# Performance work log

Measured on AMD Instinct MI355X. Metric: run time of the kernel, lower is better.

## Reference

```python
import jax, jax.numpy as jnp
import numpy as np

EPS = 1e-5
D_MODEL = 128; D_INNER = 256; D_STATE = 64; D_CONV = 4; NHEADS = 8; HEADDIM = 32
N_LAYERS = 4; PATCH = 16; IMG = 512; BATCH = 16
D_IN_PROJ = 2 * D_INNER + 2 * D_STATE + NHEADS  # 648
CONV_DIM = D_INNER + 2 * D_STATE               # 384


def _layernorm(x, g, b):
    m = jnp.mean(x, -1, keepdims=True)
    v = jnp.mean((x - m) ** 2, -1, keepdims=True)
    return (x - m) * jax.lax.rsqrt(v + EPS) * g + b


def _mamba2(x, in_w, conv_w, conv_b, dt_bias, A_log, D_skip, norm_w, out_w):
    # x: (b, l, d_model). Faithful to mamba-ssm Mamba2 (ngroups=1, rmsnorm gated, D skip).
    b, l, _ = x.shape
    zxbcdt = jnp.einsum('bld,ed->ble', x, in_w)            # (b,l,648)
    z = zxbcdt[..., :D_INNER]
    xBC = zxbcdt[..., D_INNER:D_INNER + CONV_DIM]
    dt = zxbcdt[..., -NHEADS:]
    # causal depthwise conv1d (kernel D_CONV) + SiLU
    xpad = jnp.pad(xBC, ((0, 0), (D_CONV - 1, 0), (0, 0)))
    xc = conv_b + sum(xpad[:, k:k + l, :] * conv_w[:, k] for k in range(D_CONV))
    xc = jax.nn.silu(xc)
    xs = xc[..., :D_INNER]
    B = xc[..., D_INNER:D_INNER + D_STATE]                 # (b,l,n)
    C = xc[..., -D_STATE:]                                 # (b,l,n)
    dt = jax.nn.softplus(dt + dt_bias)                     # (b,l,h)
    dA = jnp.exp(dt * (-jnp.exp(A_log)))                   # (b,l,h)
    xh = xs.reshape(b, l, NHEADS, HEADDIM)                 # (b,l,h,p)

    def step(hstate, t):
        dA_t, dt_t, B_t, x_t, C_t = t
        hstate = hstate * dA_t[:, :, None, None] + jnp.einsum('bh,bn,bhp->bhpn', dt_t, B_t, x_t)
        return hstate, jnp.einsum('bhpn,bn->bhp', hstate, C_t)

    h0 = jnp.zeros((b, NHEADS, HEADDIM, D_STATE), x.dtype)
    _, ys = jax.lax.scan(step, h0, (dA.swapaxes(0, 1), dt.swapaxes(0, 1), B.swapaxes(0, 1), xh.swapaxes(0, 1), C.swapaxes(0, 1)))
    y = ys.swapaxes(0, 1) + D_skip[None, None, :, None] * xh
    y = y.reshape(b, l, D_INNER)
    y = y * jax.nn.silu(z)                                 # gate
    y = y * jax.lax.rsqrt(jnp.mean(y * y, -1, keepdims=True) + EPS) * norm_w  # gated RMSNorm
    return jnp.einsum('ble,de->bld', y, out_w)


def _forward(x, patch_w, patch_b, pe_g, pe_b, in_w, conv_w, conv_b, dt_bias, A_log,
             D_skip, ssm_norm_w, out_w, ln_g, ln_b, fn_g, fn_b, attn_w1, attn_b1, attn_w2, attn_b2):
    b = x.shape[0]
    Hp = x.shape[2] // PATCH; Wp = x.shape[3] // PATCH
    # patch-embed conv (stride==kernel) as a reshape + einsum
    xp = x.reshape(b, 3, Hp, PATCH, Wp, PATCH)
    tok = jnp.einsum('bchpwq,dcpq->bhwd', xp, patch_w) + patch_b
    tok = tok.reshape(b, Hp * Wp, D_MODEL)
    tok = _layernorm(tok, pe_g, pe_b)
    for i in range(N_LAYERS):
        res = tok
        tok = _layernorm(tok, ln_g[i], ln_b[i])
        tok = _mamba2(tok, in_w[i], conv_w[i], conv_b[i], dt_bias[i], A_log[i],
                      D_skip[i], ssm_norm_w[i], out_w[i])
        tok = tok + res
    tok = _layernorm(tok, fn_g, fn_b)
    # attention pooling
    h1 = jnp.tanh(jnp.einsum('bld,hd->blh', tok, attn_w1) + attn_b1)
    scores = jnp.einsum('blh,oh->blo', h1, attn_w2) + attn_b2
    w = jax.nn.softmax(scores, axis=1)
    pooled = jnp.sum(w * tok, axis=1)
    nrm = jnp.maximum(jnp.sqrt(jnp.sum(pooled * pooled, -1, keepdims=True)), 1e-12)
    return pooled / nrm


def setup_inputs() -> dict:
    key = jax.random.key(0)
    ks = jax.random.split(key, 16)
    n = lambda k, shape, s=0.02: (jax.random.normal(k, shape) * s).astype(jnp.float32)
    return {
        'x': jax.random.normal(ks[0], (BATCH, 3, IMG, IMG), jnp.float32),
        'patch_w': n(ks[1], (D_MODEL, 3, PATCH, PATCH)),
        'patch_b': jnp.zeros((D_MODEL,), jnp.float32),
        'pe_g': jnp.ones((D_MODEL,), jnp.float32),
        'pe_b': jnp.zeros((D_MODEL,), jnp.float32),
        'in_w': n(ks[2], (N_LAYERS, D_IN_PROJ, D_MODEL)),
        'conv_w': n(ks[3], (N_LAYERS, CONV_DIM, D_CONV), 0.1),
        'conv_b': jnp.zeros((N_LAYERS, CONV_DIM), jnp.float32),
        'dt_bias': n(ks[4], (N_LAYERS, NHEADS), 0.5),
        'A_log': jnp.log(jax.random.uniform(ks[5], (N_LAYERS, NHEADS), jnp.float32, 1.0, 16.0)),
        'D_skip': jnp.ones((N_LAYERS, NHEADS), jnp.float32),
        'ssm_norm_w': jnp.ones((N_LAYERS, D_INNER), jnp.float32),
        'out_w': n(ks[6], (N_LAYERS, D_MODEL, D_INNER)),
        'ln_g': jnp.ones((N_LAYERS, D_MODEL), jnp.float32),
        'ln_b': jnp.zeros((N_LAYERS, D_MODEL), jnp.float32),
        'fn_g': jnp.ones((D_MODEL,), jnp.float32),
        'fn_b': jnp.zeros((D_MODEL,), jnp.float32),
        'attn_w1': n(ks[7], (D_MODEL // 2, D_MODEL), 0.05),
        'attn_b1': jnp.zeros((D_MODEL // 2,), jnp.float32),
        'attn_w2': n(ks[8], (1, D_MODEL // 2), 0.05),
        'attn_b2': jnp.zeros((1,), jnp.float32),
    }


def reference(x, patch_w, patch_b, pe_g, pe_b, in_w, conv_w, conv_b, dt_bias, A_log,
              D_skip, ssm_norm_w, out_w, ln_g, ln_b, fn_g, fn_b, attn_w1, attn_b1, attn_w2, attn_b2):
    return _forward(x, patch_w, patch_b, pe_g, pe_b, in_w, conv_w, conv_b, dt_bias, A_log,
                    D_skip, ssm_norm_w, out_w, ln_g, ln_b, fn_g, fn_b, attn_w1, attn_b1, attn_w2, attn_b2)
```

## Files before the change

kernel.cpp:

```cpp
#include <hip/hip_runtime.h>
#include <math.h>

#define EPS 1e-5f

constexpr int NB      = 16;
constexpr int L       = 1024;
constexpr int DM      = 128;
constexpr int DI      = 256;
constexpr int DS      = 64;
constexpr int NH      = 8;
constexpr int DPROJ   = 648;
constexpr int CDIM    = 384;
constexpr int EPAD    = 656;

typedef __attribute__((ext_vector_type(8))) short short8v;
typedef __attribute__((ext_vector_type(4))) float f32x4;
typedef unsigned short ushort_t;

__device__ __forceinline__ float silu_f(float x){ return x / (1.f + expf(-x)); }
__device__ __forceinline__ ushort_t f2bf(float f){
  union { float f; unsigned int u; } v; v.f = f;
  unsigned int r = v.u + 0x7FFF + ((v.u >> 16) & 1);
  return (ushort_t)(r >> 16);
}
__device__ __forceinline__ short8v pack8(float4 a, float4 b){
  short8v v;
  v[0]=(short)f2bf(a.x); v[1]=(short)f2bf(a.y); v[2]=(short)f2bf(a.z); v[3]=(short)f2bf(a.w);
  v[4]=(short)f2bf(b.x); v[5]=(short)f2bf(b.y); v[6]=(short)f2bf(b.z); v[7]=(short)f2bf(b.w);
  return v;
}

__global__ __launch_bounds__(256) void k_cvt(const float* __restrict__ in_w,
    const float* __restrict__ ln_g, const float* __restrict__ ln_b,
    const float* __restrict__ out_w, const float* __restrict__ nw,
    const float* __restrict__ patch_w, const float* __restrict__ w1,
    ushort_t* __restrict__ inwb, ushort_t* __restrict__ owb,
    ushort_t* __restrict__ pwb, float* __restrict__ biasin,
    ushort_t* __restrict__ w1b){
  const int R1 = 4 * EPAD * 128, R2 = 4 * 128 * 256, R3 = 128 * 768, R4 = 4 * EPAD, R5 = 64 * 128;
  int i = blockIdx.x * 256 + threadIdx.x;
  if (i < R1) {
    int ly = i / (EPAD * 128), rem = i % (EPAD * 128), e = rem >> 7, d = rem & 127;
    float v = 0.f;
    if (e < DPROJ) v = in_w[((size_t)ly * DPROJ + e) * 128 + d] * ln_g[ly * 128 + d];
    inwb[i] = f2bf(v);
    return;
  }
  i -= R1;
  if (i < R2) {
    int ly = i >> 15, rem = i & 32767, e = rem & 255;
    owb[i] = f2bf(out_w[i] * nw[ly * 256 + e]);
    return;
  }
  i -= R2;
  if (i < R3) { pwb[i] = f2bf(patch_w[i]); return; }
  i -= R3;
  if (i < R4) {
    int ly = i / EPAD, e = i % EPAD;
    float s = 0.f;
    if (e < DPROJ) {
      const float* r = in_w + ((size_t)ly * DPROJ + e) * 128;
      const float* b = ln_b + ly * 128;
      for (int d = 0; d < 128; ++d) s += r[d] * b[d];
    }
    biasin[i] = s;
    return;
  }
  i -= R4;
  if (i < R5) w1b[i] = f2bf(w1[i]);
}

__global__ __launch_bounds__(256) void k_patch(const float* __restrict__ x,
    const ushort_t* __restrict__ pwb, const float* __restrict__ pb,
    const float* __restrict__ pg, const float* __restrict__ pbe,
    float* __restrict__ tok){
  __shared__ ushort_t Al[64 * 128];
  __shared__ ushort_t Bl[128 * 128];
  __shared__ float spb[128], spg[128], spe[128];
  const int m0 = blockIdx.x * 64;
  const int tid = threadIdx.x;
  char* Ab = (char*)Al; char* Bb = (char*)Bl;
  if (tid < 128) { spb[tid] = pb[tid]; spg[tid] = pg[tid]; spe[tid] = pbe[tid]; }
  const int w = tid >> 6, l = tid & 63, lr = l & 15, lgp = l >> 4;
  f32x4 acc[8];
#pragma unroll
  for (int nt = 0; nt < 8; ++nt) acc[nt] = (f32x4){0.f, 0.f, 0.f, 0.f};
  for (int kc = 0; kc < 6; ++kc) {
    __syncthreads();
    for (int idx = tid; idx < 128 * 16; idx += 256) {
      int n = idx >> 4, ch = idx & 15;
      short8v v = *(const short8v*)(pwb + (size_t)n * 768 + kc * 128 + (ch << 3));
      *(short8v*)(Bb + n * 256 + ((ch * 16) ^ ((n & 7) << 4))) = v;
    }
    {
      const int c = kc >> 1;
      for (int i = tid; i < 1024; i += 256) {
        int t = i >> 4, p = (i >> 1) & 7, o = i & 1;
        int T = m0 + t, bb = T >> 10, tl = T & 1023, hp = tl >> 5, wp = tl & 31;
        const float* src = x + (((size_t)(bb * 3 + c) * 512 + hp * 16 + ((kc & 1) << 3) + p) * 512
                                + wp * 16 + o * 8);
        float4 f0 = *(const float4*)src;
        float4 f1 = *(const float4*)(src + 4);
        short8v v = pack8(f0, f1);
        int kk = p * 16 + o * 8;
        *(short8v*)(Ab + t * 256 + ((kk * 2) ^ ((t & 7) << 4))) = v;
      }
// ... 39 lines not shown
      tok[row + col] = (v - mean) * rstd * spg[col] + spe[col];
    }
  }
}

__global__ __launch_bounds__(256) void k_inproj(const float* __restrict__ tok,
    const ushort_t* __restrict__ inwb, const float* __restrict__ biasin,
    float* __restrict__ zx){
  __shared__ ushort_t Al[128 * 128];
  __shared__ ushort_t Bl[176 * 128];
  __shared__ float sBias[176];
  const int blk = blockIdx.x;
  const int mb = blk >> 2, nb = blk & 3;
  const int m0 = mb << 7, n0 = nb * 176;
  const int NT = (nb == 3) ? 128 : 176;
  const int tid = threadIdx.x;
  char* Ab = (char*)Al; char* Bb = (char*)Bl;
  for (int idx = tid; idx < (NT << 4); idx += 256) {
    int row = idx >> 4, ch = idx & 15;
    short8v v = *(const short8v*)(inwb + ((size_t)(n0 + row) << 7) + (ch << 3));
    *(short8v*)(Bb + row * 256 + ((ch * 16) ^ ((row & 7) << 4))) = v;
  }
  for (int idx = tid; idx < NT; idx += 256) sBias[idx] = biasin[n0 + idx];
  for (int rp = 0; rp < 2; ++rp) {
    const int r = (rp << 6) + (tid >> 2), t4 = tid & 3;
    const float* src = tok + (((size_t)(m0 + r)) << 7) + t4 * 32;
    float v[32];
    float s = 0.f, sq = 0.f;
#pragma unroll
    for (int k = 0; k < 8; ++k) {
      float4 f = *(const float4*)(src + 4 * k);
      v[4*k] = f.x; v[4*k+1] = f.y; v[4*k+2] = f.z; v[4*k+3] = f.w;
      s += f.x + f.y + f.z + f.w;
      sq += f.x*f.x + f.y*f.y + f.z*f.z + f.w*f.w;
    }
    s  += __shfl_xor(s, 1, 4);  s  += __shfl_xor(s, 2, 4);
    sq += __shfl_xor(sq, 1, 4); sq += __shfl_xor(sq, 2, 4);
    float mean = s * (1.f / 128.f);
    float var  = sq * (1.f / 128.f) - mean * mean;
    float rstd = rsqrtf(var + EPS);
#pragma unroll
    for (int k = 0; k < 4; ++k) {
      short8v o;
#pragma unroll
      for (int e = 0; e < 8; ++e) o[e] = (short)f2bf((v[8*k + e] - mean) * rstd);
      *(short8v*)(Ab + r * 256 + ((t4 * 64 + 16 * k) ^ ((r & 7) << 4))) = o;
    }
  }
  __syncthreads();
  const int w = tid >> 6, l = tid & 63, lr = l & 15, lgp = l >> 4;
  const int xsl = (lr & 7) << 4;
  short8v a[2][4];
#pragma unroll
  for (int mi = 0; mi < 2; ++mi) {
    const int mt = w + mi * 4;
#pragma unroll
    for (int ks = 0; ks < 4; ++ks)
      a[mi][ks] = *(const short8v*)(Ab + (16 * mt + lr) * 256 + ((ks * 64 + lgp * 16) ^ xsl));
  }
  const int NTT = NT >> 4;
  for (int nt = 0; nt < NTT; ++nt) {
    f32x4 acc0 = (f32x4){0.f, 0.f, 0.f, 0.f};
    f32x4 acc1 = (f32x4){0.f, 0.f, 0.f, 0.f};
#pragma unroll
    for (int ks = 0; ks < 4; ++ks) {
      short8v b = *(const short8v*)(Bb + (nt * 16 + lr) * 256 + ((ks * 64 + lgp * 16) ^ xsl));
      acc0 = __builtin_amdgcn_mfma_f32_16x16x32_bf16(a[0][ks], b, acc0, 0, 0, 0);
      acc1 = __builtin_amdgcn_mfma_f32_16x16x32_bf16(a[1][ks], b, acc1, 0, 0, 0);
    }
    const int col = n0 + nt * 16 + lr;
    if (col < DPROJ) {
      const float bias = sBias[nt * 16 + lr];
#pragma unroll
      for (int r = 0; r < 4; ++r) {
        zx[((size_t)(m0 + 16 * w       + lgp * 4 + r)) * DPROJ + col] = acc0[r] + bias;
        zx[((size_t)(m0 + 16 * (w + 4) + lgp * 4 + r)) * DPROJ + col] = acc1[r] + bias;
      }
    }
  }
}

constexpr int CONVC = 192;
__global__ __launch_bounds__(256) void k_conv(const float* __restrict__ zx,
    const float* __restrict__ cw, const float* __restrict__ cb, float* __restrict__ xc){
  __shared__ float st[67][CONVC];
  __shared__ float swt[CONVC][4];
  __shared__ float sbias[CONVC];
  const int blk = blockIdx.x;
  const int cg = blk & 1, tile = (blk >> 1) & 15, b = blk >> 5;
  const int l0 = tile << 6, ch0 = cg * CONVC;
  const int tid = threadIdx.x;
  for (int i = tid; i < CONVC; i += 256) {
    float4 wv = *(const float4*)(cw + (size_t)(ch0 + i) * 4);
    swt[i][0] = wv.x; swt[i][1] = wv.y; swt[i][2] = wv.z; swt[i][3] = wv.w;
    sbias[i] = cb[ch0 + i];
  }
  for (int i = tid; i < 67 * 48; i += 256) {
    int rr = i / 48, q4 = i % 48;
    int lrow = l0 + rr - 3;
    float4 v = make_float4(0.f, 0.f, 0.f, 0.f);
    if (lrow >= 0) v = *(const float4*)(zx + ((size_t)(b << 10) + lrow) * DPROJ + DI + ch0 + q4 * 4);
    *(float4*)(&st[rr][q4 * 4]) = v;
  }
  __syncthreads();
  for (int i = tid; i < 64 * CONVC; i += 256) {
    int t = i / CONVC, c2 = i % CONVC;
    float acc = sbias[c2] + st[t][c2] * swt[c2][0] + st[t+1][c2] * swt[c2][1]
              + st[t+2][c2] * swt[c2][2] + st[t+3][c2] * swt[c2][3];
    acc = silu_f(acc);
    xc[((size_t)(b << 10) + l0 + t) * CDIM + ch0 + c2] = acc;
  }
}

__global__ __launch_bounds__(64) void k_dt(const float* __restrict__ zx,
    const float* __restrict__ dtbias, const float* __restrict__ Alog,
    float* __restrict__ dtb, float* __restrict__ lcb, float* __restrict__ Acb){
  const int blk = blockIdx.x;
  const int c = blk & 15, h = (blk >> 4) & 7, b = blk >> 7;
  const int s = threadIdx.x;
  const int l = (c << 6) + s;
  float raw = zx[((size_t)(b << 10) + l) * DPROJ + 640 + h] + dtbias[h];
  float dt = raw > 20.f ? raw : log1pf(expf(raw));
  float la = dt * (-expf(Alog[h]));
  float cum = la;
  for (int off = 1; off < 64; off <<= 1) {
    float v = __shfl_up(cum, off, 64);
    if (s >= off) cum += v;
  }
  size_t o = ((size_t)((b << 3) + h) << 10) + l;
  dtb[o] = dt; lcb[o] = cum;
  if (s == 63) Acb[blk] = expf(cum);
}

__global__ __launch_bounds__(256) void k_cstate(const float* __restrict__ xc,
    const float* __restrict__ dtb, const float* __restrict__ lcb,
    float* __restrict__ Sc){
  __shared__ ushort_t sXc[32 * 64];
  __shared__ ushort_t sBt[64 * 64];
  __shared__ float scoef[64];
  const int blk = blockIdx.x;
  const int c = blk & 15, h = (blk >> 4) & 7, b = blk >> 7;
  const int tid = threadIdx.x;
  const int l0 = c << 6;
  char* pA = (char*)sXc; char* pB = (char*)sBt;
  const size_t obh = ((size_t)((b << 3) + h) << 10) + l0;
  if (tid < 64) {
    float lcT = lcb[obh + 63];
    scoef[tid] = dtb[obh + tid] * __expf(fminf(lcT - lcb[obh + tid], 0.f));
  }
  const int s = tid >> 2, q = tid & 3;
  const size_t rowb = ((size_t)(b << 10) + l0 + s) * CDIM;
  float4 b0 = *(const float4*)(xc + rowb + DI + q * 16);
  float4 b1 = *(const float4*)(xc + rowb + DI + q * 16 + 4);
  float4 b2 = *(const float4*)(xc + rowb + DI + q * 16 + 8);
  float4 b3 = *(const float4*)(xc + rowb + DI + q * 16 + 12);
  float4 x0 = *(const float4*)(xc + rowb + (h << 5) + q * 8);
  float4 x1 = *(const float4*)(xc + rowb + (h << 5) + q * 8 + 4);
  float bv[16] = {b0.x,b0.y,b0.z,b0.w, b1.x,b1.y,b1.z,b1.w,
                  b2.x,b2.y,b2.z,b2.w, b3.x,b3.y,b3.z,b3.w};
#pragma unroll
  for (int j = 0; j < 16; ++j) {
    const int n = q * 16 + j;
    *(ushort_t*)(pB + n * 128 + ((s * 2) ^ ((n & 7) << 4))) = f2bf(bv[j]);
  }
  __syncthreads();
  const float cf = scoef[s];
  float xv[8] = {x0.x,x0.y,x0.z,x0.w, x1.x,x1.y,x1.z,x1.w};
#pragma unroll
  for (int j = 0; j < 8; ++j) {
    const int p = q * 8 + j;
    *(ushort_t*)(pA + p * 128 + ((s * 2) ^ ((p & 7) << 4))) = f2bf(cf * xv[j]);
  }
  __syncthreads();
  const int w = tid >> 6, l = tid & 63, lr = l & 15, lgp = l >> 4;
  const int xsl = (lr & 7) << 4;
  const int pt = w & 1, ng = w >> 1;
  short8v a0 = *(const short8v*)(pA + (pt * 16 + lr) * 128 + ((lgp * 16) ^ xsl));
  short8v a1 = *(const short8v*)(pA + (pt * 16 + lr) * 128 + ((64 + lgp * 16) ^ xsl));
  float* dst = Sc + ((size_t)blk << 11);
#pragma unroll
  for (int ni = 0; ni < 2; ++ni) {
    const int nt = ng * 2 + ni;
    f32x4 acc = (f32x4){0.f, 0.f, 0.f, 0.f};
    short8v bb0 = *(const short8v*)(pB + (nt * 16 + lr) * 128 + ((lgp * 16) ^ xsl));
    short8v bb1 = *(const short8v*)(pB + (nt * 16 + lr) * 128 + ((64 + lgp * 16) ^ xsl));
    acc = __builtin_amdgcn_mfma_f32_16x16x32_bf16(a0, bb0, acc, 0, 0, 0);
    acc = __builtin_amdgcn_mfma_f32_16x16x32_bf16(a1, bb1, acc, 0, 0, 0);
#pragma unroll
    for (int r = 0; r < 4; ++r)
      dst[(pt * 16 + lgp * 4 + r) * 64 + nt * 16 + lr] = acc[r];
  }
}

__global__ __launch_bounds__(256) void k_hscan(float* __restrict__ Sc, const float* __restrict__ Acb){
  const int blk = blockIdx.x;
  const int bh = blk >> 3;
  const int e = ((blk & 7) << 8) + threadIdx.x;
  float hs = 0.f;
  const size_t base = ((size_t)bh << 15) + e;
  for (int c = 0; c < 16; ++c) {
    const size_t o = base + ((size_t)c << 11);
    float v = Sc[o];
    Sc[o] = hs;
    hs = Acb[(bh << 4) + c] * hs + v;
  }
}

__global__ __launch_bounds__(256) void k_chunky(const float* __restrict__ xc,
    const float* __restrict__ h0buf, const float* __restrict__ dtb,
    const float* __restrict__ lcb, const float* __restrict__ Dsk,
    float* __restrict__ ys){
  __shared__ ushort_t sC[64 * 64];
  __shared__ ushort_t sBm[64 * 64];
  __shared__ ushort_t sAW[64 * 128];
  __shared__ ushort_t sBX[32 * 128];
  __shared__ float sXT[32][65];
  __shared__ float sdt[64], slc[64];
  const int blk = blockIdx.x;
  const int c = blk & 15, h = (blk >> 4) & 7, b = blk >> 7;
  const int tid = threadIdx.x;
  const int l0 = c << 6;
  char* pC = (char*)sC; char* pB = (char*)sBm; char* pA = (char*)sAW; char* pX = (char*)sBX;
  const size_t obh = ((size_t)((b << 3) + h) << 10) + l0;
  if (tid < 64) { sdt[tid] = dtb[obh + tid]; slc[tid] = lcb[obh + tid]; }
  {
    const int row = tid >> 2, q = tid & 3;
    const size_t rowb = ((size_t)(b << 10) + l0 + row) * CDIM;
    const float Pt = __expf(lcb[obh + row]);
    const int xs = (row & 7) << 4;
    float4 b0 = *(const float4*)(xc + rowb + DI + q * 16);
    float4 b1 = *(const float4*)(xc + rowb + DI + q * 16 + 4);
    float4 b2 = *(const float4*)(xc + rowb + DI + q * 16 + 8);
    float4 b3 = *(const float4*)(xc + rowb + DI + q * 16 + 12);
    *(short8v*)(pB + row * 128 + ((q * 32) ^ xs))      = pack8(b0, b1);
    *(short8v*)(pB + row * 128 + ((q * 32 + 16) ^ xs)) = pack8(b2, b3);
    float4 c0 = *(const float4*)(xc + rowb + DI + DS + q * 16);
    float4 c1 = *(const float4*)(xc + rowb + DI + DS + q * 16 + 4);
    float4 c2 = *(const float4*)(xc + rowb + DI + DS + q * 16 + 8);
    float4 c3 = *(const float4*)(xc + rowb + DI + DS + q * 16 + 12);
    *(short8v*)(pC + row * 128 + ((q * 32) ^ xs))      = pack8(c0, c1);
    *(short8v*)(pC + row * 128 + ((q * 32 + 16) ^ xs)) = pack8(c2, c3);
    float4 p0 = make_float4(c0.x*Pt, c0.y*Pt, c0.z*Pt, c0.w*Pt);
    float4 p1 = make_float4(c1.x*Pt, c1.y*Pt, c1.z*Pt, c1.w*Pt);
    float4 p2 = make_float4(c2.x*Pt, c2.y*Pt, c2.z*Pt, c2.w*Pt);
    float4 p3 = make_float4(c3.x*Pt, c3.y*Pt, c3.z*Pt, c3.w*Pt);
    *(short8v*)(pA + row * 256 + ((128 + q * 32) ^ xs))      = pack8(p0, p1);
    *(short8v*)(pA + row * 256 + ((128 + q * 32 + 16) ^ xs)) = pack8(p2, p3);
    float4 x0 = *(const float4*)(xc + rowb + (h << 5) + q * 8);
    float4 x1 = *(const float4*)(xc + rowb + (h << 5) + q * 8 + 4);
    sXT[q*8+0][row] = x0.x; sXT[q*8+1][row] = x0.y; sXT[q*8+2][row] = x0.z; sXT[q*8+3][row] = x0.w;
    sXT[q*8+4][row] = x1.x; sXT[q*8+5][row] = x1.y; sXT[q*8+6][row] = x1.z; sXT[q*8+7][row] = x1.w;
  }
  {
    const int p = tid >> 3, n8 = (tid & 7) << 3;
    float4 h0a = *(const float4*)(h0buf + ((size_t)blk << 11) + (p << 6) + n8);
    float4 h0b = *(const float4*)(h0buf + ((size_t)blk << 11) + (p << 6) + n8 + 4);
    *(short8v*)(pX + p * 256 + (((64 + n8) * 2) ^ ((p & 7) << 4))) = pack8(h0a, h0b);
  }
  __syncthreads();
  {
    const int p = tid >> 3, s8 = (tid & 7) << 3;
    short8v vx;
#pragma unroll
    for (int e = 0; e < 8; ++e) vx[e] = (short)f2bf(sXT[p][s8 + e]);
    *(short8v*)(pX + p * 256 + ((s8 * 2) ^ ((p & 7) << 4))) = vx;
  }
  const int w = tid >> 6, l = tid & 63, lr = l & 15, lgp = l >> 4;
  const int xsl = (lr & 7) << 4;
  f32x4 accg[4];
#pragma unroll
  for (int nt = 0; nt < 4; ++nt) accg[nt] = (f32x4){0.f, 0.f, 0.f, 0.f};
  {
    short8v a0 = *(const short8v*)(pC + (16 * w + lr) * 128 + ((lgp * 16) ^ xsl));
    short8v a1 = *(const short8v*)(pC + (16 * w + lr) * 128 + ((64 + lgp * 16) ^ xsl));
#pragma unroll
    for (int nt = 0; nt < 4; ++nt) {
      short8v b0 = *(const short8v*)(pB + (nt * 16 + lr) * 128 + ((lgp * 16) ^ xsl));
      short8v b1 = *(const short8v*)(pB + (nt * 16 + lr) * 128 + ((64 + lgp * 16) ^ xsl));
      accg[nt] = __builtin_amdgcn_mfma_f32_16x16x32_bf16(a0, b0, accg[nt], 0, 0, 0);
      accg[nt] = __builtin_amdgcn_mfma_f32_16x16x32_bf16(a1, b1, accg[nt], 0, 0, 0);
    }
  }
#pragma unroll
  for (int nt = 0; nt < 4; ++nt) {
    const int s = nt * 16 + lr;
    const float ds = sdt[s], ls = slc[s];
#pragma unroll
    for (int r = 0; r < 4; ++r) {
      const int t = 16 * w + lgp * 4 + r;
      float wv = 0.f;
      if (s <= t) wv = ds * __expf(fminf(slc[t] - ls, 0.f)) * accg[nt][r];
      *(ushort_t*)(pA + t * 256 + ((s * 2) ^ ((t & 7) << 4))) = f2bf(wv);
    }
  }
  __syncthreads();
  f32x4 accy[2];
  accy[0] = (f32x4){0.f, 0.f, 0.f, 0.f};
  accy[1] = (f32x4){0.f, 0.f, 0.f, 0.f};
  short8v aw[4];
#pragma unroll
  for (int ks = 0; ks < 4; ++ks)
    aw[ks] = *(const short8v*)(pA + (16 * w + lr) * 256 + ((ks * 64 + lgp * 16) ^ xsl));
#pragma unroll
  for (int nt = 0; nt < 2; ++nt) {
#pragma unroll
    for (int ks = 0; ks < 4; ++ks) {
      short8v bx = *(const short8v*)(pX + (nt * 16 + lr) * 256 + ((ks * 64 + lgp * 16) ^ xsl));
      accy[nt] = __builtin_amdgcn_mfma_f32_16x16x32_bf16(aw[ks], bx, accy[nt], 0, 0, 0);
    }
  }
  const float dsk = Dsk[h];
#pragma unroll
  for (int nt = 0; nt < 2; ++nt) {
    const int p = nt * 16 + lr;
#pragma unroll
    for (int r = 0; r < 4; ++r) {
      const int t = 16 * w + lgp * 4 + r;
      ys[((size_t)(b << 10) + l0 + t) * DI + (h << 5) + p] = accy[nt][r] + dsk * sXT[p][t];
    }
  }
}

__global__ __launch_bounds__(256) void k_gateout(const float* __restrict__ zx,
    const float* __restrict__ ys, const ushort_t* __restrict__ owb,
    float* __restrict__ tok){
  __shared__ ushort_t Al[64 * 256];
  __shared__ ushort_t Bl[128 * 64];
  const int m0 = blockIdx.x * 64;
  const int tid = threadIdx.x;
  char* Ab = (char*)Al; char* Bb = (char*)Bl;
  {
    const int r = tid >> 2, t4 = tid & 3;
    const size_t row = (size_t)(m0 + r);
    const float* yp = ys + row * 256 + t4 * 64;
    const float* zp = zx + row * DPROJ + t4 * 64;
    float p[64];
    float sq = 0.f;
#pragma unroll
    for (int k = 0; k < 16; ++k) {
      float4 fy = *(const float4*)(yp + 4 * k);
      float4 fz = *(const float4*)(zp + 4 * k);
      float a0 = fy.x * (fz.x / (1.f + __expf(-fz.x)));
      float a1 = fy.y * (fz.y / (1.f + __expf(-fz.y)));
      float a2 = fy.z * (fz.z / (1.f + __expf(-fz.z)));
      float a3 = fy.w * (fz.w / (1.f + __expf(-fz.w)));
      p[4*k] = a0; p[4*k+1] = a1; p[4*k+2] = a2; p[4*k+3] = a3;
      sq += a0*a0 + a1*a1 + a2*a2 + a3*a3;
    }
    sq += __shfl_xor(sq, 1, 4); sq += __shfl_xor(sq, 2, 4);
    float rstd = rsqrtf(sq * (1.f / 256.f) + EPS);
#pragma unroll
    for (int k = 0; k < 8; ++k) {
      short8v o;
#pragma unroll
      for (int e = 0; e < 8; ++e) o[e] = (short)f2bf(p[8*k + e] * rstd);
      *(short8v*)(Ab + r * 512 + ((t4 * 128 + 16 * k) ^ ((r & 7) << 4))) = o;
    }
  }
  const int w = tid >> 6, l = tid & 63, lr = l & 15, lgp = l >> 4;
  f32x4 acc[8];
#pragma unroll
  for (int nt = 0; nt < 8; ++nt) acc[nt] = (f32x4){0.f, 0.f, 0.f, 0.f};
  for (int kq = 0; kq < 4; ++kq) {
    __syncthreads();
    for (int idx = tid; idx < 128 * 8; idx += 256) {
      int row = idx >> 3, ch = idx & 7;
      short8v v = *(const short8v*)(owb + ((size_t)row << 8) + kq * 64 + (ch << 3));
      *(short8v*)(Bb + row * 128 + ((ch * 16) ^ ((row & 7) << 4))) = v;
    }
    __syncthreads();
    short8v a0 = *(const short8v*)(Ab + (16*w + lr) * 512 + ((kq * 128 +      lgp * 16) ^ ((lr & 7) << 4)));
    short8v a1 = *(const short8v*)(Ab + (16*w + lr) * 512 + ((kq * 128 + 64 + lgp * 16) ^ ((lr & 7) << 4)));
#pragma unroll
    for (int nt = 0; nt < 8; ++nt) {
      short8v b0 = *(const short8v*)(Bb + (nt * 16 + lr) * 128 + ((     lgp * 16) ^ ((lr & 7) << 4)));
      short8v b1 = *(const short8v*)(Bb + (nt * 16 + lr) * 128 + ((64 + lgp * 16) ^ ((lr & 7) << 4)));
      acc[nt] = __builtin_amdgcn_mfma_f32_16x16x32_bf16(a0, b0, acc[nt], 0, 0, 0);
      acc[nt] = __builtin_amdgcn_mfma_f32_16x16x32_bf16(a1, b1, acc[nt], 0, 0, 0);
    }
  }
#pragma unroll
  for (int nt = 0; nt < 8; ++nt) {
#pragma unroll
    for (int r = 0; r < 4; ++r) {
      tok[((size_t)(m0 + 16 * w + lgp * 4 + r)) * 128 + nt * 16 + lr] += acc[nt][r];
    }
  }
}

__global__ __launch_bounds__(256) void k_score(const float* __restrict__ tok,
    const float* __restrict__ fg, const float* __restrict__ fb,
    const ushort_t* __restrict__ w1b, const float* __restrict__ b1,
    const float* __restrict__ w2, const float* __restrict__ b2,
    float* __restrict__ tokF, float* __restrict__ sc){
  __shared__ ushort_t Al[64 * 128];
  __shared__ ushort_t Wl[64 * 128];
  __shared__ float sb1[64], sw2[64];
  const int m0 = blockIdx.x * 64;
  const int tid = threadIdx.x;
  char* Ab = (char*)Al; char* Wb = (char*)Wl;
  for (int idx = tid; idx < 64 * 16; idx += 256) {
    int row = idx >> 4, ch = idx & 15;
    short8v v = *(const short8v*)(w1b + (row << 7) + (ch << 3));
    *(short8v*)(Wb + row * 256 + ((ch * 16) ^ ((row & 7) << 4))) = v;
  }
  if (tid < 64) { sb1[tid] = b1[tid]; sw2[tid] = w2[tid]; }
  {
    const int r = tid >> 2, t4 = tid & 3;
    const float* src = tok + (((size_t)(m0 + r)) << 7) + t4 * 32;
    float v[32];
    float s = 0.f, sq = 0.f;
#pragma unroll
    for (int k = 0; k < 8; ++k) {
      float4 f = *(const float4*)(src + 4 * k);
      v[4*k] = f.x; v[4*k+1] = f.y; v[4*k+2] = f.z; v[4*k+3] = f.w;
      s += f.x + f.y + f.z + f.w;
      sq += f.x*f.x + f.y*f.y + f.z*f.z + f.w*f.w;
    }
    s  += __shfl_xor(s, 1, 4);  s  += __shfl_xor(s, 2, 4);
    sq += __shfl_xor(sq, 1, 4); sq += __shfl_xor(sq, 2, 4);
    float mean = s * (1.f / 128.f);
    float var  = sq * (1.f / 128.f) - mean * mean;
    float rstd = rsqrtf(var + EPS);
    float* tdst = tokF + (((size_t)(m0 + r)) << 7) + t4 * 32;
#pragma unroll
    for (int k = 0; k < 4; ++k) {
      float o8[8];
      float4 g0 = *(const float4*)(fg + t4 * 32 + 8 * k);
      float4 g1 = *(const float4*)(fg + t4 * 32 + 8 * k + 4);
      float4 e0 = *(const float4*)(fb + t4 * 32 + 8 * k);
// ... 33 lines not shown
#pragma unroll
  for (int r = 0; r < 4; ++r) {
    for (int off = 1; off < 16; off <<= 1) sacc[r] += __shfl_xor(sacc[r], off, 16);
  }
  if (lr == 0) {
    const float bb2 = b2[0];
#pragma unroll
    for (int r = 0; r < 4; ++r) sc[m0 + 16 * w + lgp * 4 + r] = sacc[r] + bb2;
  }
}

__global__ __launch_bounds__(256) void k_pool1(const float* __restrict__ tokF,
    const float* __restrict__ sc, float* __restrict__ pp){
  __shared__ float sw[128];
  __shared__ float sacc[128];
  __shared__ float sse[2];
  const int bs = blockIdx.x, b = bs >> 3, seg = bs & 7, tid = threadIdx.x;
  const int l0 = (b << 10) + (seg << 7);
  if (tid < 128) sw[tid] = __expf(sc[l0 + tid]);
  __syncthreads();
  const int d = tid & 127, g = tid >> 7;
  const float* tf = tokF + ((size_t)(l0 + (g << 6))) * 128 + d;
  float acc = 0.f;
#pragma unroll 4
  for (int i = 0; i < 64; ++i) acc += sw[(g << 6) + i] * tf[(size_t)i * 128];
  if (g == 0) sacc[d] = acc;
  float e = (tid < 128) ? sw[tid] : 0.f;
  for (int off = 32; off; off >>= 1) e += __shfl_xor(e, off);
  if ((tid & 63) == 0 && tid < 128) sse[tid >> 6] = e;
  __syncthreads();
  if (g == 1) pp[bs * 132 + d] = sacc[d] + acc;
  if (tid == 0) pp[bs * 132 + 128] = sse[0] + sse[1];
}

__global__ __launch_bounds__(128) void k_pool2(const float* __restrict__ pp,
    float* __restrict__ out){
  __shared__ float s2[2];
  const int b = blockIdx.x, tid = threadIdx.x;
  float num = 0.f, den = 0.f;
#pragma unroll
  for (int seg = 0; seg < 8; ++seg) {
    num += pp[(b * 8 + seg) * 132 + tid];
    den += pp[(b * 8 + seg) * 132 + 128];
  }
  float pooled = num / den;
  float sq = pooled * pooled;
  for (int off = 32; off; off >>= 1) sq += __shfl_xor(sq, off);
  if ((tid & 63) == 0) s2[tid >> 6] = sq;
  __syncthreads();
  float nrm = fmaxf(sqrtf(s2[0] + s2[1]), 1e-12f);
  out[(size_t)b * 128 + tid] = pooled / nrm;
}

extern "C" void kernel_launch(void* const* d_in, const int* in_sizes, int n_in,
                              void* d_out, int out_size, void* d_ws, size_t ws_size,
                              hipStream_t stream) {
  const float* x       = (const float*)d_in[0];
  const float* patch_w = (const float*)d_in[1];
  const float* patch_b = (const float*)d_in[2];
  const float* pe_g    = (const float*)d_in[3];
  const float* pe_b    = (const float*)d_in[4];
  const float* in_w    = (const float*)d_in[5];
  const float* conv_w  = (const float*)d_in[6];
  const float* conv_b  = (const float*)d_in[7];
  const float* dt_bias = (const float*)d_in[8];
  const float* A_log   = (const float*)d_in[9];
  const float* D_skip  = (const float*)d_in[10];
  const float* nw      = (const float*)d_in[11];
  const float* out_w   = (const float*)d_in[12];
  const float* ln_g    = (const float*)d_in[13];
  const float* ln_b    = (const float*)d_in[14];
  const float* fn_g    = (const float*)d_in[15];
  const float* fn_b    = (const float*)d_in[16];
  const float* w1      = (const float*)d_in[17];
  const float* b1      = (const float*)d_in[18];
  const float* w2      = (const float*)d_in[19];
  const float* b2      = (const float*)d_in[20];
  float* out = (float*)d_out;
  char* ws = (char*)d_ws;

  size_t off = 0;
  float* tok  = (float*)(ws + off); off += (size_t)NB * L * DM * 4;
  float* zx   = (float*)(ws + off); off += (size_t)NB * L * DPROJ * 4;
  float* xcb  = (float*)(ws + off); off += (size_t)NB * L * CDIM * 4;
  float* ysb  = (float*)(ws + off); off += (size_t)NB * L * DI * 4;
  float* Scb  = (float*)(ws + off); off += (size_t)NB * NH * 16 * 2048 * 4;
  float* dtb  = (float*)(ws + off); off += (size_t)NB * NH * L * 4;
  float* lcb  = (float*)(ws + off); off += (size_t)NB * NH * L * 4;
  float* Acb  = (float*)(ws + off); off += (size_t)NB * NH * 16 * 4;
  ushort_t* inwb = (ushort_t*)(ws + off); off += (size_t)4 * EPAD * 128 * 2;
  ushort_t* owb  = (ushort_t*)(ws + off); off += (size_t)4 * 128 * 256 * 2;
  ushort_t* pwb  = (ushort_t*)(ws + off); off += (size_t)128 * 768 * 2;
  float* biasin  = (float*)(ws + off); off += (size_t)4 * EPAD * 4;
  ushort_t* w1b  = (ushort_t*)(ws + off); off += (size_t)64 * 128 * 2;
  float* pp      = (float*)(ws + off); off += (size_t)128 * 132 * 4;
  float* tokF = zx;
  float* scb  = (float*)(ws + (size_t)30 * 1024 * 1024);

  {
    const int total = 4 * EPAD * 128 + 4 * 128 * 256 + 128 * 768 + 4 * EPAD + 64 * 128;
    k_cvt<<<(total + 255) / 256, 256, 0, stream>>>(in_w, ln_g, ln_b, out_w, nw, patch_w, w1,
                                                   inwb, owb, pwb, biasin, w1b);
  }
  k_patch<<<256, 256, 0, stream>>>(x, pwb, patch_b, pe_g, pe_b, tok);
  for (int ly = 0; ly < 4; ++ly) {
    k_inproj<<<512, 256, 0, stream>>>(tok, inwb + (size_t)ly * EPAD * 128,
                                      biasin + ly * EPAD, zx);
    k_conv<<<NB * 16 * 2, 256, 0, stream>>>(zx, conv_w + (size_t)ly * CDIM * 4,
                                            conv_b + ly * CDIM, xcb);
    k_dt<<<NB * NH * 16, 64, 0, stream>>>(zx, dt_bias + ly * NH, A_log + ly * NH,
                                          dtb, lcb, Acb);
    k_cstate<<<NB * NH * 16, 256, 0, stream>>>(xcb, dtb, lcb, Scb);
    k_hscan<<<NB * NH * 8, 256, 0, stream>>>(Scb, Acb);
    k_chunky<<<NB * NH * 16, 256, 0, stream>>>(xcb, Scb, dtb, lcb,
                                               D_skip + ly * NH, ysb);
    k_gateout<<<256, 256, 0, stream>>>(zx, ysb, owb + (size_t)ly * 128 * 256, tok);
  }
  k_score<<<256, 256, 0, stream>>>(tok, fn_g, fn_b, w1b, b1, w2, b2, tokF, scb);
  k_pool1<<<128, 256, 0, stream>>>(tokF, scb, pp);
  k_pool2<<<16, 128, 0, stream>>>(pp, out);
}
```

Before: 513.8 us.

## Fuse SSD chunk kernels into one sequential-chunk kernel with bf16 intermediates

Replaces the four SSD kernels (dt/cumsum, chunk state, inter-chunk scan, chunk output) with a single kernel per (batch, head, half-head) that walks the 16 chunks in order. It keeps the running state in registers and prefetches the next chunk's inputs. The conv output and the SSM output are now stored as bf16 instead of fp32, which halves that memory traffic and removes the Sc/dt/lc workspace round trips and three launches. The trade-off is far fewer blocks (256 instead of 2048) with a serial chunk loop, which lowers parallelism and lengthens the critical path. The inter-chunk state is also now rounded to bf16 before its matmul.

```diff
diff --git a/kernel.cpp b/kernel.cpp
--- a/kernel.cpp
+++ b/kernel.cpp
@@ -14,6 +14,7 @@
 constexpr int EPAD    = 656;
 
 typedef __attribute__((ext_vector_type(8))) short short8v;
+typedef __attribute__((ext_vector_type(4))) short short4v;
 typedef __attribute__((ext_vector_type(4))) float f32x4;
 typedef unsigned short ushort_t;
 
@@ -22,6 +23,10 @@
   union { float f; unsigned int u; } v; v.f = f;
   unsigned int r = v.u + 0x7FFF + ((v.u >> 16) & 1);
   return (ushort_t)(r >> 16);
+}
+__device__ __forceinline__ float bf2f(ushort_t u){
+  union { float f; unsigned int u; } v; v.u = ((unsigned int)u) << 16;
+  return v.f;
 }
 __device__ __forceinline__ short8v pack8(float4 a, float4 b){
   short8v v;
@@ -227,7 +232,7 @@
 
 constexpr int CONVC = 192;
 __global__ __launch_bounds__(256) void k_conv(const float* __restrict__ zx,
-    const float* __restrict__ cw, const float* __restrict__ cb, float* __restrict__ xc){
+    const float* __restrict__ cw, const float* __restrict__ cb, ushort_t* __restrict__ xc){
   __shared__ float st[67][CONVC];
   __shared__ float swt[CONVC][4];
   __shared__ float sbias[CONVC];
@@ -248,226 +253,173 @@
     *(float4*)(&st[rr][q4 * 4]) = v;
   }
   __syncthreads();
-  for (int i = tid; i < 64 * CONVC; i += 256) {
-    int t = i / CONVC, c2 = i % CONVC;
-    float acc = sbias[c2] + st[t][c2] * swt[c2][0] + st[t+1][c2] * swt[c2][1]
-              + st[t+2][c2] * swt[c2][2] + st[t+3][c2] * swt[c2][3];
-    acc = silu_f(acc);
-    xc[((size_t)(b << 10) + l0 + t) * CDIM + ch0 + c2] = acc;
-  }
-}
-
-__global__ __launch_bounds__(64) void k_dt(const float* __restrict__ zx,
-    const float* __restrict__ dtbias, const float* __restrict__ Alog,
-    float* __restrict__ dtb, float* __restrict__ lcb, float* __restrict__ Acb){
-  const int blk = blockIdx.x;
-  const int c = blk & 15, h = (blk >> 4) & 7, b = blk >> 7;
-  const int s = threadIdx.x;
-  const int l = (c << 6) + s;
-  float raw = zx[((size_t)(b << 10) + l) * DPROJ + 640 + h] + dtbias[h];
-  float dt = raw > 20.f ? raw : log1pf(expf(raw));
-  float la = dt * (-expf(Alog[h]));
-  float cum = la;
-  for (int off = 1; off < 64; off <<= 1) {
-    float v = __shfl_up(cum, off, 64);
-    if (s >= off) cum += v;
-  }
-  size_t o = ((size_t)((b << 3) + h) << 10) + l;
-  dtb[o] = dt; lcb[o] = cum;
-  if (s == 63) Acb[blk] = expf(cum);
-}
-
-__global__ __launch_bounds__(256) void k_cstate(const float* __restrict__ xc,
-    const float* __restrict__ dtb, const float* __restrict__ lcb,
-    float* __restrict__ Sc){
-  __shared__ ushort_t sXc[32 * 64];
-  __shared__ ushort_t sBt[64 * 64];
-  __shared__ float scoef[64];
-  const int blk = blockIdx.x;
-  const int c = blk & 15, h = (blk >> 4) & 7, b = blk >> 7;
-  const int tid = threadIdx.x;
-  const int l0 = c << 6;
-  char* pA = (char*)sXc; char* pB = (char*)sBt;
-  const size_t obh = ((size_t)((b << 3) + h) << 10) + l0;
-  if (tid < 64) {
-    float lcT = lcb[obh + 63];
-    scoef[tid] = dtb[obh + tid] * __expf(fminf(lcT - lcb[obh + tid], 0.f));
-  }
-  const int s = tid >> 2, q = tid & 3;
-  const size_t rowb = ((size_t)(b << 10) + l0 + s) * CDIM;
-  float4 b0 = *(const float4*)(xc + rowb + DI + q * 16);
-  float4 b1 = *(const float4*)(xc + rowb + DI + q * 16 + 4);
-  float4 b2 = *(const float4*)(xc + rowb + DI + q * 16 + 8);
-  float4 b3 = *(const float4*)(xc + rowb + DI + q * 16 + 12);
-  float4 x0 = *(const float4*)(xc + rowb + (h << 5) + q * 8);
-  float4 x1 = *(const float4*)(xc + rowb + (h << 5) + q * 8 + 4);
-  float bv[16] = {b0.x,b0.y,b0.z,b0.w, b1.x,b1.y,b1.z,b1.w,
-                  b2.x,b2.y,b2.z,b2.w, b3.x,b3.y,b3.z,b3.w};
-#pragma unroll
-  for (int j = 0; j < 16; ++j) {
-    const int n = q * 16 + j;
-    *(ushort_t*)(pB + n * 128 + ((s * 2) ^ ((n & 7) << 4))) = f2bf(bv[j]);
-  }
-  __syncthreads();
-  const float cf = scoef[s];
-  float xv[8] = {x0.x,x0.y,x0.z,x0.w, x1.x,x1.y,x1.z,x1.w};
-#pragma unroll
-  for (int j = 0; j < 8; ++j) {
-    const int p = q * 8 + j;
-    *(ushort_t*)(pA + p * 128 + ((s * 2) ^ ((p & 7) << 4))) = f2bf(cf * xv[j]);
-  }
-  __syncthreads();
-  const int w = tid >> 6, l = tid & 63, lr = l & 15, lgp = l >> 4;
-  const int xsl = (lr & 7) << 4;
-  const int pt = w & 1, ng = w >> 1;
-  short8v a0 = *(const short8v*)(pA + (pt * 16 + lr) * 128 + ((lgp * 16) ^ xsl));
-  short8v a1 = *(const short8v*)(pA + (pt * 16 + lr) * 128 + ((64 + lgp * 16) ^ xsl));
-  float* dst = Sc + ((size_t)blk << 11);
-#pragma unroll
-  for (int ni = 0; ni < 2; ++ni) {
-    const int nt = ng * 2 + ni;
-    f32x4 acc = (f32x4){0.f, 0.f, 0.f, 0.f};
-    short8v bb0 = *(const short8v*)(pB + (nt * 16 + lr) * 128 + ((lgp * 16) ^ xsl));
-    short8v bb1 = *(const short8v*)(pB + (nt * 16 + lr) * 128 + ((64 + lgp * 16) ^ xsl));
-    acc = __builtin_amdgcn_mfma_f32_16x16x32_bf16(a0, bb0, acc, 0, 0, 0);
-    acc = __builtin_amdgcn_mfma_f32_16x16x32_bf16(a1, bb1, acc, 0, 0, 0);
-#pragma unroll
-    for (int r = 0; r < 4; ++r)
-      dst[(pt * 16 + lgp * 4 + r) * 64 + nt * 16 + lr] = acc[r];
-  }
-}
-
-__global__ __launch_bounds__(256) void k_hscan(float* __restrict__ Sc, const float* __restrict__ Acb){
-  const int blk = blockIdx.x;
-  const int bh = blk >> 3;
-  const int e = ((blk & 7) << 8) + threadIdx.x;
-  float hs = 0.f;
-  const size_t base = ((size_t)bh << 15) + e;
-  for (int c = 0; c < 16; ++c) {
-    const size_t o = base + ((size_t)c << 11);
-    float v = Sc[o];
-    Sc[o] = hs;
-    hs = Acb[(bh << 4) + c] * hs + v;
-  }
-}
-
-__global__ __launch_bounds__(256) void k_chunky(const float* __restrict__ xc,
-    const float* __restrict__ h0buf, const float* __restrict__ dtb,
-    const float* __restrict__ lcb, const float* __restrict__ Dsk,
-    float* __restrict__ ys){
-  __shared__ ushort_t sC[64 * 64];
+  for (int i = tid; i < 64 * 48; i += 256) {
+    int t = i / 48, g = i % 48;
+    short4v ov;
+#pragma unroll
+    for (int j = 0; j < 4; ++j) {
+      int c2 = g * 4 + j;
+      float acc = sbias[c2] + st[t][c2] * swt[c2][0] + st[t+1][c2] * swt[c2][1]
+                + st[t+2][c2] * swt[c2][2] + st[t+3][c2] * swt[c2][3];
+      ov[j] = (short)f2bf(silu_f(acc));
+    }
+    *(short4v*)(xc + ((size_t)(b << 10) + l0 + t) * CDIM + ch0 + g * 4) = ov;
+  }
+}
+
+__global__ __launch_bounds__(256) void k_ssd(const ushort_t* __restrict__ xcb,
+    const float* __restrict__ zx, const float* __restrict__ dtbias,
+    const float* __restrict__ Alog, const float* __restrict__ Dsk,
+    ushort_t* __restrict__ ys){
   __shared__ ushort_t sBm[64 * 64];
+  __shared__ ushort_t sCm[64 * 64];
+  __shared__ ushort_t sBT[64 * 64];
   __shared__ ushort_t sAW[64 * 128];
-  __shared__ ushort_t sBX[32 * 128];
-  __shared__ float sXT[32][65];
+  __shared__ ushort_t sBX[16 * 128];
   __shared__ float sdt[64], slc[64];
   const int blk = blockIdx.x;
-  const int c = blk & 15, h = (blk >> 4) & 7, b = blk >> 7;
+  const int ph = blk & 1, h = (blk >> 1) & 7, b = blk >> 4;
   const int tid = threadIdx.x;
-  const int l0 = c << 6;
-  char* pC = (char*)sC; char* pB = (char*)sBm; char* pA = (char*)sAW; char* pX = (char*)sBX;
-  const size_t obh = ((size_t)((b << 3) + h) << 10) + l0;
-  if (tid < 64) { sdt[tid] = dtb[obh + tid]; slc[tid] = lcb[obh + tid]; }
+  const int w = tid >> 6, l = tid & 63, lr = l & 15, lgp = l >> 4;
+  char* pB = (char*)sBm; char* pC = (char*)sCm; char* pT = (char*)sBT;
+  char* pA = (char*)sAW; char* pX = (char*)sBX;
+  const int srow = tid >> 2, sq = tid & 3;
+  const int xs = (srow & 7) << 4;
+  const int xsl = (lr & 7) << 4;
+  const float dtb_h = dtbias[h];
+  const float nA = -expf(Alog[h]);
+  const float dsk = Dsk[h];
+  const size_t base_b = (size_t)(b << 10);
+  float hfrag[4] = {0.f, 0.f, 0.f, 0.f};
+  short8v pb0, pb1, pc0, pc1; short4v px; float dtraw = 0.f;
   {
-    const int row = tid >> 2, q = tid & 3;
-    const size_t rowb = ((size_t)(b << 10) + l0 + row) * CDIM;
-    const float Pt = __expf(lcb[obh + row]);
-    const int xs = (row & 7) << 4;
-    float4 b0 = *(const float4*)(xc + rowb + DI + q * 16);
-    float4 b1 = *(const float4*)(xc + rowb + DI + q * 16 + 4);
-    float4 b2 = *(const float4*)(xc + rowb + DI + q * 16 + 8);
-    float4 b3 = *(const float4*)(xc + rowb + DI + q * 16 + 12);
-    *(short8v*)(pB + row * 128 + ((q * 32) ^ xs))      = pack8(b0, b1);
-    *(short8v*)(pB + row * 128 + ((q * 32 + 16) ^ xs)) = pack8(b2, b3);
-    float4 c0 = *(const float4*)(xc + rowb + DI + DS + q * 16);
-    float4 c1 = *(const float4*)(xc + rowb + DI + DS + q * 16 + 4);
-    float4 c2 = *(const float4*)(xc + rowb + DI + DS + q * 16 + 8);
-    float4 c3 = *(const float4*)(xc + rowb + DI + DS + q * 16 + 12);
-    *(short8v*)(pC + row * 128 + ((q * 32) ^ xs))      = pack8(c0, c1);
-    *(short8v*)(pC + row * 128 + ((q * 32 + 16) ^ xs)) = pack8(c2, c3);
-    float4 p0 = make_float4(c0.x*Pt, c0.y*Pt, c0.z*Pt, c0.w*Pt);
-    float4 p1 = make_float4(c1.x*Pt, c1.y*Pt, c1.z*Pt, c1.w*Pt);
-    float4 p2 = make_float4(c2.x*Pt, c2.y*Pt, c2.z*Pt, c2.w*Pt);
-    float4 p3 = make_float4(c3.x*Pt, c3.y*Pt, c3.z*Pt, c3.w*Pt);
-    *(short8v*)(pA + row * 256 + ((128 + q * 32) ^ xs))      = pack8(p0, p1);
-    *(short8v*)(pA + row * 256 + ((128 + q * 32 + 16) ^ xs)) = pack8(p2, p3);
-    float4 x0 = *(const float4*)(xc + rowb + (h << 5) + q * 8);
-    float4 x1 = *(const float4*)(xc + rowb + (h << 5) + q * 8 + 4);
-    sXT[q*8+0][row] = x0.x; sXT[q*8+1][row] = x0.y; sXT[q*8+2][row] = x0.z; sXT[q*8+3][row] = x0.w;
-    sXT[q*8+4][row] = x1.x; sXT[q*8+5][row] = x1.y; sXT[q*8+6][row] = x1.z; sXT[q*8+7][row] = x1.w;
-  }
-  {
-    const int p = tid >> 3, n8 = (tid & 7) << 3;
-    float4 h0a = *(const float4*)(h0buf + ((size_t)blk << 11) + (p << 6) + n8);
-    float4 h0b = *(const float4*)(h0buf + ((size_t)blk << 11) + (p << 6) + n8 + 4);
-    *(short8v*)(pX + p * 256 + (((64 + n8) * 2) ^ ((p & 7) << 4))) = pack8(h0a, h0b);
-  }
-  __syncthreads();
-  {
-    const int p = tid >> 3, s8 = (tid & 7) << 3;
-    short8v vx;
-#pragma unroll
-    for (int e = 0; e < 8; ++e) vx[e] = (short)f2bf(sXT[p][s8 + e]);
-    *(short8v*)(pX + p * 256 + ((s8 * 2) ^ ((p & 7) << 4))) = vx;
-  }
-  const int w = tid >> 6, l = tid & 63, lr = l & 15, lgp = l >> 4;
-  const int xsl = (lr & 7) << 4;
-  f32x4 accg[4];
-#pragma unroll
-  for (int nt = 0; nt < 4; ++nt) accg[nt] = (f32x4){0.f, 0.f, 0.f, 0.f};
-  {
-    short8v a0 = *(const short8v*)(pC + (16 * w + lr) * 128 + ((lgp * 16) ^ xsl));
-    short8v a1 = *(const short8v*)(pC + (16 * w + lr) * 128 + ((64 + lgp * 16) ^ xsl));
-#pragma unroll
-    for (int nt = 0; nt < 4; ++nt) {
-      short8v b0 = *(const short8v*)(pB + (nt * 16 + lr) * 128 + ((lgp * 16) ^ xsl));
-      short8v b1 = *(const short8v*)(pB + (nt * 16 + lr) * 128 + ((64 + lgp * 16) ^ xsl));
-      accg[nt] = __builtin_amdgcn_mfma_f32_16x16x32_bf16(a0, b0, accg[nt], 0, 0, 0);
-      accg[nt] = __builtin_amdgcn_mfma_f32_16x16x32_bf16(a1, b1, accg[nt], 0, 0, 0);
-    }
-  }
-#pragma unroll
-  for (int nt = 0; nt < 4; ++nt) {
-    const int s = nt * 16 + lr;
-    const float ds = sdt[s], ls = slc[s];
+    const ushort_t* xr = xcb + (base_b + srow) * CDIM;
+    pb0 = *(const short8v*)(xr + 256 + sq * 16);
+    pb1 = *(const short8v*)(xr + 256 + sq * 16 + 8);
+    pc0 = *(const short8v*)(xr + 320 + sq * 16);
+    pc1 = *(const short8v*)(xr + 320 + sq * 16 + 8);
+    px  = *(const short4v*)(xr + (h << 5) + (ph << 4) + sq * 4);
+    if (tid < 64) dtraw = zx[(base_b + tid) * DPROJ + 640 + h];
+  }
+  for (int c = 0; c < 16; ++c) {
+    const int l0 = c << 6;
+    *(short8v*)(pB + srow * 128 + ((sq * 32) ^ xs))      = pb0;
+    *(short8v*)(pB + srow * 128 + ((sq * 32 + 16) ^ xs)) = pb1;
+    *(short8v*)(pC + srow * 128 + ((sq * 32) ^ xs))      = pc0;
+    *(short8v*)(pC + srow * 128 + ((sq * 32 + 16) ^ xs)) = pc1;
+#pragma unroll
+    for (int j = 0; j < 4; ++j) {
+      const int p = sq * 4 + j;
+      *(ushort_t*)(pX + p * 256 + ((srow * 2) ^ ((p & 7) << 4))) = (ushort_t)px[j];
+    }
 #pragma unroll
     for (int r = 0; r < 4; ++r) {
-      const int t = 16 * w + lgp * 4 + r;
-      float wv = 0.f;
-      if (s <= t) wv = ds * __expf(fminf(slc[t] - ls, 0.f)) * accg[nt][r];
-      *(ushort_t*)(pA + t * 256 + ((s * 2) ^ ((t & 7) << 4))) = f2bf(wv);
-    }
-  }
-  __syncthreads();
-  f32x4 accy[2];
-  accy[0] = (f32x4){0.f, 0.f, 0.f, 0.f};
-  accy[1] = (f32x4){0.f, 0.f, 0.f, 0.f};
-  short8v aw[4];
-#pragma unroll
-  for (int ks = 0; ks < 4; ++ks)
-    aw[ks] = *(const short8v*)(pA + (16 * w + lr) * 256 + ((ks * 64 + lgp * 16) ^ xsl));
-#pragma unroll
-  for (int nt = 0; nt < 2; ++nt) {
+      const int p = lgp * 4 + r, n = (w << 4) + lr;
+      *(ushort_t*)(pX + p * 256 + ((128 + n * 2) ^ ((p & 7) << 4))) = f2bf(hfrag[r]);
+    }
+    if (tid < 64) {
+      float raw = dtraw + dtb_h;
+      float dt = raw > 20.f ? raw : log1pf(expf(raw));
+      float cum = dt * nA;
+      for (int off = 1; off < 64; off <<= 1) {
+        float v = __shfl_up(cum, off, 64);
+        if (tid >= off) cum += v;
+      }
+      sdt[tid] = dt; slc[tid] = cum;
+    }
+    __syncthreads();
+    const float lcT = slc[63];
+    {
+      const float coef = sdt[srow] * __expf(fminf(lcT - slc[srow], 0.f));
+#pragma unroll
+      for (int j = 0; j < 16; ++j) {
+        const int n = sq * 16 + j;
+        float bvf = bf2f((ushort_t)(j < 8 ? pb0[j] : pb1[j - 8]));
+        *(ushort_t*)(pT + n * 128 + ((srow * 2) ^ ((n & 7) << 4))) = f2bf(coef * bvf);
+      }
+      const float Pt = __expf(slc[srow]);
+      short8v q0, q1;
+#pragma unroll
+      for (int j = 0; j < 8; ++j) {
+        q0[j] = (short)f2bf(Pt * bf2f((ushort_t)pc0[j]));
+        q1[j] = (short)f2bf(Pt * bf2f((ushort_t)pc1[j]));
+      }
+      *(short8v*)(pA + srow * 256 + ((128 + sq * 32) ^ xs))      = q0;
+      *(short8v*)(pA + srow * 256 + ((128 + sq * 32 + 16) ^ xs)) = q1;
+    }
+    f32x4 accg[4];
+#pragma unroll
+    for (int nt = 0; nt < 4; ++nt) accg[nt] = (f32x4){0.f, 0.f, 0.f, 0.f};
+    {
+      short8v a0 = *(const short8v*)(pC + ((w << 4) + lr) * 128 + ((lgp * 16) ^ xsl));
+      short8v a1 = *(const short8v*)(pC + ((w << 4) + lr) * 128 + ((64 + lgp * 16) ^ xsl));
+#pragma unroll
+      for (int nt = 0; nt < 4; ++nt) {
+        short8v b0 = *(const short8v*)(pB + (nt * 16 + lr) * 128 + ((lgp * 16) ^ xsl));
+        short8v b1 = *(const short8v*)(pB + (nt * 16 + lr) * 128 + ((64 + lgp * 16) ^ xsl));
+        accg[nt] = __builtin_amdgcn_mfma_f32_16x16x32_bf16(a0, b0, accg[nt], 0, 0, 0);
+        accg[nt] = __builtin_amdgcn_mfma_f32_16x16x32_bf16(a1, b1, accg[nt], 0, 0, 0);
+      }
+    }
+    __syncthreads();
+    {
+      short8v xa0 = *(const short8v*)(pX + lr * 256 + ((lgp * 16) ^ xsl));
+      short8v xa1 = *(const short8v*)(pX + lr * 256 + ((64 + lgp * 16) ^ xsl));
+      short8v bt0 = *(const short8v*)(pT + ((w << 4) + lr) * 128 + ((lgp * 16) ^ xsl));
+      short8v bt1 = *(const short8v*)(pT + ((w << 4) + lr) * 128 + ((64 + lgp * 16) ^ xsl));
+      f32x4 S = (f32x4){0.f, 0.f, 0.f, 0.f};
+      S = __builtin_amdgcn_mfma_f32_16x16x32_bf16(xa0, bt0, S, 0, 0, 0);
+      S = __builtin_amdgcn_mfma_f32_16x16x32_bf16(xa1, bt1, S, 0, 0, 0);
+      const float Ac = __expf(lcT);
+#pragma unroll
+      for (int r = 0; r < 4; ++r) hfrag[r] = Ac * hfrag[r] + S[r];
+    }
+    {
+      float lct_r[4];
+#pragma unroll
+      for (int r = 0; r < 4; ++r) lct_r[r] = slc[(w << 4) + lgp * 4 + r];
+#pragma unroll
+      for (int nt = 0; nt < 4; ++nt) {
+        const int s = nt * 16 + lr;
+        const float ds = sdt[s], ls = slc[s];
+#pragma unroll
+        for (int r = 0; r < 4; ++r) {
+          const int t = (w << 4) + lgp * 4 + r;
+          float wv = 0.f;
+          if (s <= t) wv = ds * __expf(fminf(lct_r[r] - ls, 0.f)) * accg[nt][r];
+          *(ushort_t*)(pA + t * 256 + ((s * 2) ^ ((t & 7) << 4))) = f2bf(wv);
+        }
+      }
+    }
+    __syncthreads();
+    if (c < 15) {
+      const ushort_t* xr = xcb + (base_b + l0 + 64 + srow) * CDIM;
+      pb0 = *(const short8v*)(xr + 256 + sq * 16);
+      pb1 = *(const short8v*)(xr + 256 + sq * 16 + 8);
+      pc0 = *(const short8v*)(xr + 320 + sq * 16);
+      pc1 = *(const short8v*)(xr + 320 + sq * 16 + 8);
+      px  = *(const short4v*)(xr + (h << 5) + (ph << 4) + sq * 4);
+      if (tid < 64) dtraw = zx[(base_b + l0 + 64 + tid) * DPROJ + 640 + h];
+    }
+    f32x4 accy = (f32x4){0.f, 0.f, 0.f, 0.f};
 #pragma unroll
     for (int ks = 0; ks < 4; ++ks) {
-      short8v bx = *(const short8v*)(pX + (nt * 16 + lr) * 256 + ((ks * 64 + lgp * 16) ^ xsl));
-      accy[nt] = __builtin_amdgcn_mfma_f32_16x16x32_bf16(aw[ks], bx, accy[nt], 0, 0, 0);
-    }
-  }
-  const float dsk = Dsk[h];
-#pragma unroll
-  for (int nt = 0; nt < 2; ++nt) {
-    const int p = nt * 16 + lr;
+      short8v aw = *(const short8v*)(pA + ((w << 4) + lr) * 256 + ((ks * 64 + lgp * 16) ^ xsl));
+      short8v bx = *(const short8v*)(pX + lr * 256 + ((ks * 64 + lgp * 16) ^ xsl));
+      accy = __builtin_amdgcn_mfma_f32_16x16x32_bf16(aw, bx, accy, 0, 0, 0);
+    }
 #pragma unroll
     for (int r = 0; r < 4; ++r) {
-      const int t = 16 * w + lgp * 4 + r;
-      ys[((size_t)(b << 10) + l0 + t) * DI + (h << 5) + p] = accy[nt][r] + dsk * sXT[p][t];
-    }
+      const int t = (w << 4) + lgp * 4 + r;
+      float xv = bf2f(*(const ushort_t*)(pX + lr * 256 + ((t * 2) ^ xsl)));
+      ys[(base_b + l0 + t) * DI + (h << 5) + (ph << 4) + lr] = f2bf(accy[r] + dsk * xv);
+    }
+    __syncthreads();
   }
 }
 
 __global__ __launch_bounds__(256) void k_gateout(const float* __restrict__ zx,
-    const float* __restrict__ ys, const ushort_t* __restrict__ owb,
+    const ushort_t* __restrict__ ysb, const ushort_t* __restrict__ owb,
     float* __restrict__ tok){
   __shared__ ushort_t Al[64 * 256];
   __shared__ ushort_t Bl[128 * 64];
@@ -477,20 +429,21 @@
   {
     const int r = tid >> 2, t4 = tid & 3;
     const size_t row = (size_t)(m0 + r);
-    const float* yp = ys + row * 256 + t4 * 64;
+    const ushort_t* yp = ysb + row * 256 + t4 * 64;
     const float* zp = zx + row * DPROJ + t4 * 64;
     float p[64];
     float sq = 0.f;
 #pragma unroll
-    for (int k = 0; k < 16; ++k) {
-      float4 fy = *(const float4*)(yp + 4 * k);
-      float4 fz = *(const float4*)(zp + 4 * k);
-      float a0 = fy.x * (fz.x / (1.f + __expf(-fz.x)));
-      float a1 = fy.y * (fz.y / (1.f + __expf(-fz.y)));
-      float a2 = fy.z * (fz.z / (1.f + __expf(-fz.z)));
-      float a3 = fy.w * (fz.w / (1.f + __expf(-fz.w)));
-      p[4*k] = a0; p[4*k+1] = a1; p[4*k+2] = a2; p[4*k+3] = a3;
-      sq += a0*a0 + a1*a1 + a2*a2 + a3*a3;
+    for (int k = 0; k < 8; ++k) {
+      short8v y8 = *(const short8v*)(yp + 8 * k);
+      float4 fz0 = *(const float4*)(zp + 8 * k);
+      float4 fz1 = *(const float4*)(zp + 8 * k + 4);
+      float zz[8] = {fz0.x, fz0.y, fz0.z, fz0.w, fz1.x, fz1.y, fz1.z, fz1.w};
+#pragma unroll
+      for (int j = 0; j < 8; ++j) {
+        float a = bf2f((ushort_t)y8[j]) * (zz[j] / (1.f + __expf(-zz[j])));
+        p[8 * k + j] = a; sq += a * a;
+      }
     }
     sq += __shfl_xor(sq, 1, 4); sq += __shfl_xor(sq, 2, 4);
     float rstd = rsqrtf(sq * (1.f / 256.f) + EPS);
@@ -690,12 +643,8 @@
   size_t off = 0;
   float* tok  = (float*)(ws + off); off += (size_t)NB * L * DM * 4;
   float* zx   = (float*)(ws + off); off += (size_t)NB * L * DPROJ * 4;
-  float* xcb  = (float*)(ws + off); off += (size_t)NB * L * CDIM * 4;
-  float* ysb  = (float*)(ws + off); off += (size_t)NB * L * DI * 4;
-  float* Scb  = (float*)(ws + off); off += (size_t)NB * NH * 16 * 2048 * 4;
-  float* dtb  = (float*)(ws + off); off += (size_t)NB * NH * L * 4;
-  float* lcb  = (float*)(ws + off); off += (size_t)NB * NH * L * 4;
-  float* Acb  = (float*)(ws + off); off += (size_t)NB * NH * 16 * 4;
+  ushort_t* xcb = (ushort_t*)(ws + off); off += (size_t)NB * L * CDIM * 2;
+  ushort_t* ysb = (ushort_t*)(ws + off); off += (size_t)NB * L * DI * 2;
   ushort_t* inwb = (ushort_t*)(ws + off); off += (size_t)4 * EPAD * 128 * 2;
   ushort_t* owb  = (ushort_t*)(ws + off); off += (size_t)4 * 128 * 256 * 2;
   ushort_t* pwb  = (ushort_t*)(ws + off); off += (size_t)128 * 768 * 2;
@@ -716,12 +665,8 @@
                                       biasin + ly * EPAD, zx);
     k_conv<<<NB * 16 * 2, 256, 0, stream>>>(zx, conv_w + (size_t)ly * CDIM * 4,
                                             conv_b + ly * CDIM, xcb);
-    k_dt<<<NB * NH * 16, 64, 0, stream>>>(zx, dt_bias + ly * NH, A_log + ly * NH,
-                                          dtb, lcb, Acb);
-    k_cstate<<<NB * NH * 16, 256, 0, stream>>>(xcb, dtb, lcb, Scb);
-    k_hscan<<<NB * NH * 8, 256, 0, stream>>>(Scb, Acb);
-    k_chunky<<<NB * NH * 16, 256, 0, stream>>>(xcb, Scb, dtb, lcb,
-                                               D_skip + ly * NH, ysb);
+    k_ssd<<<NB * NH * 2, 256, 0, stream>>>(xcb, zx, dt_bias + ly * NH,
+                                           A_log + ly * NH, D_skip + ly * NH, ysb);
     k_gateout<<<256, 256, 0, stream>>>(zx, ysb, owb + (size_t)ly * 128 * 256, tok);
   }
   k_score<<<256, 256, 0, stream>>>(tok, fn_g, fn_b, w1b, b1, w2, b2, tokF, scb);
```

After: 558.1 us. 8.6% more time.
